# Optimization experiments

Hardware: AMD Instinct MI355X
Metric: run time of the kernel (lower is better)

Reference implementation:

```python
import jax, jax.numpy as jnp
import numpy as np

H, V, B, S = 2048, 32000, 16, 256

def setup_inputs() -> dict:
    key = jax.random.key(0)
    k1, k2, k3, k4 = jax.random.split(key, 4)
    # Parameters exactly as the torch __init__ builds them
    alpha_exp = jax.nn.softmax(jax.random.normal(k1, (H, H), dtype=jnp.float32), axis=1)   # transition probs [H,H]
    beta = jax.nn.log_softmax(jax.random.normal(k2, (H, V), dtype=jnp.float32), axis=1)    # emission log-probs [H,V]
    gamma = jax.nn.log_softmax(jax.random.normal(k3, (H,), dtype=jnp.float32), axis=0)     # initial-state logits [H]
    input_ids = jax.random.randint(k4, (B, S), 0, V)
    return {"input_ids": input_ids, "alpha_exp": alpha_exp, "beta": beta, "gamma": gamma}


def _hmm_forward(input_ids, alpha_exp, beta, gamma):
    # gamma stored as log-probs; forward re-softmaxes it (faithful to torch code)
    gamma_exp = jax.nn.softmax(gamma)                       # [H]
    ids = input_ids.T                                       # [S,B]
    mask = (ids != -1).astype(beta.dtype)                   # [S,B]; -1 = padding
    # input_probs[t,h,b] = beta[h, ids[t,b]] * mask
    ip = jnp.transpose(beta[:, ids], (1, 0, 2)) * mask[:, None, :]   # [S,H,B]
    ip_rev = ip[::-1]                                       # process t = S-1 .. 0

    def step(y, ipt):
        # log-domain backward recursion: y' = log(alpha_exp @ exp(y - ymax)) + ymax + emission
        ymax = jnp.max(y, axis=0, keepdims=True)            # [1,B]
        y = jnp.log(alpha_exp @ jnp.exp(y - ymax)) + ymax + ipt
        return y, y

    y0 = ip_rev[0]                                          # t = S-1: y starts at 0, += emission
    y_last, ys_rest = jax.lax.scan(step, y0, ip_rev[1:])
    ys = jnp.concatenate([y0[None], ys_rest], axis=0)       # [S,H,B], ys[i] is t = S-1-i

    ymax = jnp.max(y_last, axis=0)                          # [B]
    final = jnp.log(gamma_exp @ jnp.exp(y_last - ymax[None, :])) + ymax   # [B] per-seq loglik
    return ys, final


def reference(input_ids, alpha_exp, beta, gamma):
    return _hmm_forward(input_ids, alpha_exp, beta, gamma)
```

## Files before the change

### kernel.cpp

```cpp
#include <hip/hip_runtime.h>
#include <cstdint>
#include <cstddef>

#define Hh 2048
#define Vv 32000
#define Bb 16
#define Ss 256

typedef unsigned short ushort_t;
typedef unsigned int   uint_t;
typedef unsigned long long ull_t;

typedef __attribute__((ext_vector_type(8))) short short8;
typedef __attribute__((ext_vector_type(4))) float f32x4;

#define Z_OFF    0ull
#define Z_SLOT   ((size_t)Bb * Hh * 2)
#define Z_BYTES  ((size_t)3 * Z_SLOT)
#define Y_OFF    (Z_OFF + Z_BYTES)
#define Y_BYTES  ((size_t)Bb * Hh * 4)
#define WS_NEED  (Y_OFF + Y_BYTES)

#define LD_REL(p)     __hip_atomic_load((p), __ATOMIC_RELAXED, __HIP_MEMORY_SCOPE_AGENT)
#define ST_REL(p, v)  __hip_atomic_store((p), (v), __ATOMIC_RELAXED, __HIP_MEMORY_SCOPE_AGENT)

#define SGN64 0x8000800080008000ull
#define MAG64 0x7FFF7FFF7FFF7FFFull

__device__ __forceinline__ float b2f_u(uint_t u) {
  union { uint_t u; float f; } x; x.u = u; return x.f;
}
__device__ __forceinline__ ushort_t f2b(float f) {
  union { float f; uint_t u; } x; x.f = f;
  uint_t u = x.u;
  return (ushort_t)((u + 0x7FFFu + ((u >> 16) & 1u)) >> 16);
}
__device__ __forceinline__ uint_t umaxu(uint_t a, uint_t b) { return a > b ? a : b; }
__device__ __forceinline__ uint_t pkmax16(uint_t a, uint_t b) {
  uint_t lo = umaxu(a & 0xFFFFu, b & 0xFFFFu);
  uint_t hi = umaxu(a >> 16, b >> 16);
  return lo | (hi << 16);
}

__global__ __launch_bounds__(256, 1) void hmm_persist(
    const float* __restrict__ alpha,
    const float* __restrict__ beta,
    const int*  __restrict__ ids,
    ushort_t* __restrict__ Zbuf,
    float* __restrict__ Y255,
    float* __restrict__ out)
{
  const int w    = blockIdx.x;
  const int g    = w & 7;
  const int wl   = w >> 3;
  const int c0   = g * 2;
  const int tid  = threadIdx.x;
  const int wv   = tid >> 6;
  const int lane = tid & 63;
  const int lrow = lane & 15;
  const int quad = lane >> 4;
  const int r0   = wl * 64 + wv * 16;

  __shared__ __align__(16) ushort_t zTf[2 * 2080];
  __shared__ float ybuf[128];
  __shared__ float ipld[128];
  __shared__ uint_t redm[4];

  ull_t*  Zb64 = (ull_t*)Zbuf;
  uint_t* Zb32 = (uint_t*)Zbuf;

  short8 afr[64];
  {
    const float* arow = alpha + (size_t)(r0 + lrow) * Hh + quad * 8;
    #pragma unroll
    for (int kt = 0; kt < 64; ++kt) {
      float4 f0 = *(const float4*)(arow + kt * 32);
      float4 f1 = *(const float4*)(arow + kt * 32 + 4);
      short8 fr;
      fr[0] = (short)f2b(f0.x); fr[1] = (short)f2b(f0.y);
      fr[2] = (short)f2b(f0.z); fr[3] = (short)f2b(f0.w);
      fr[4] = (short)f2b(f1.x); fr[5] = (short)f2b(f1.y);
      fr[6] = (short)f2b(f1.z); fr[7] = (short)f2b(f1.w);
      afr[kt] = fr;
    }
  }

  const int myc = tid & 1;
  const int myr = wl * 64 + (tid >> 1);
  float ipreg = 0.f;

  {
    float yv = 0.f;
    if (tid < 128) {
      const int v = ids[(c0 + myc) * Ss + (Ss - 1)];
      yv = beta[(size_t)myr * Vv + v];
      ybuf[tid] = yv;
      out[(size_t)myr * Bb + (c0 + myc)] = yv;
    }
    __syncthreads();
    if (tid < 64) {
      const int c = tid >> 5, rr0 = (tid & 31) * 2;
      uint_t lo = f2b(__expf(ybuf[rr0 * 2 + c]));
      uint_t hi = f2b(__expf(ybuf[rr0 * 2 + 2 + c]));
      ST_REL(Zb32 + (size_t)(c0 + c) * 1024 + (wl * 32 + (tid & 31)),
             lo | (hi << 16));
    }
    if (tid < 128) {
      const int v1 = ids[(c0 + myc) * Ss + (Ss - 2)];
      ipreg = beta[(size_t)myr * Vv + v1];
    }
  }

  float mprev = 0.f;
  const ushort_t* zbase = zTf + (lrow & 1) * 2080 + quad * 8;

  for (int k = 1; k < Ss; ++k) {
    const int   physR = (3 - ((k - 1) % 3)) % 3;
    const ull_t expS  = ((k - 1) & 1) ? SGN64 : 0ull;

    ull_t zr[4];
    ull_t* zp[4];
    #pragma unroll
    for (int j = 0; j < 4; ++j) {
      const int idx = j * 256 + tid;
      const int c   = idx >> 9;
      const int h4  = idx & 511;
      zp[j] = Zb64 + (size_t)physR * (Bb * 512) + (size_t)(c0 + c) * 512 + h4;
      zr[j] = LD_REL(zp[j]);
    }
    while (true) {
      int bad = 0;
      #pragma unroll
      for (int j = 0; j < 4; ++j)
        if ((zr[j] & SGN64) != expS) bad |= (1 << j);
      if (!bad) break;
      #pragma unroll
      for (int j = 0; j < 4; ++j)
        if (bad & (1 << j)) zr[j] = LD_REL(zp[j]);
    }

    uint_t mloc[2] = {0u, 0u};
    #pragma unroll
    for (int j = 0; j < 4; ++j) {
      const ull_t v = zr[j] & MAG64;
      const int idx = j * 256 + tid;
      const int c   = idx >> 9;
      const int h   = (idx & 511) * 4;
      *(ull_t*)(zTf + c * 2080 + h) = v;
      uint_t a = (uint_t)v, b = (uint_t)(v >> 32);
      uint_t m2 = pkmax16(a, b);
      mloc[j >> 1] = umaxu(mloc[j >> 1], umaxu(m2 & 0xFFFFu, m2 >> 16));
    }
    if (tid < 128) ipld[tid] = ipreg;

    uint_t pk = mloc[0] | (mloc[1] << 16);
    #pragma unroll
    for (int d = 1; d < 64; d <<= 1)
      pk = pkmax16(pk, __shfl_xor(pk, d));
    if (lane == 0) redm[wv] = pk;
    __syncthreads();

    const uint_t rr  = pkmax16(pkmax16(redm[0], redm[1]),
                               pkmax16(redm[2], redm[3]));
    const uint_t mzb = (((lrow & 1) ? (rr >> 16) : (rr & 0xFFFFu)) << 16);
    const float  lmax = __logf(b2f_u(mzb));

    if (k < Ss - 1 && tid < 128) {
      const int v = ids[(c0 + myc) * Ss + (Ss - 2 - k)];
      ipreg = beta[(size_t)myr * Vv + v];
    }

    f32x4 acc[8];
    {
      f32x4 zv = {0.f, 0.f, 0.f, 0.f};
      #pragma unroll
      for (int j = 0; j < 8; ++j) acc[j] = zv;
    }
    #pragma unroll
    for (int kt = 0; kt < 64; ++kt) {
      short8 bfr = *(const short8*)(zbase + kt * 32);
      acc[kt & 7] = __builtin_amdgcn_mfma_f32_16x16x32_bf16(afr[kt], bfr, acc[kt & 7], 0, 0, 0);
    }
    f32x4 sf = ((acc[0] + acc[1]) + (acc[2] + acc[3])) +
               ((acc[4] + acc[5]) + (acc[6] + acc[7]));

    const int  c   = lrow;
    const int  rb  = r0 + quad * 4;
    const int  lrr = wv * 16 + quad * 4;
    const bool act = (lrow < 2);
    const int   physW = (3 - (k % 3)) % 3;
    const ull_t orS   = (k & 1) ? SGN64 : 0ull;
    const float mnew  = mprev + lmax;
    if (act) {
      float yv4[4];
      #pragma unroll
      for (int i = 0; i < 4; ++i)
        yv4[i] = __logf(sf[i]) + mprev + ipld[(lrr + i) * 2 + c];
      uint_t o0 = (uint_t)f2b(__expf(yv4[0] - mnew)) |
                  ((uint_t)f2b(__expf(yv4[1] - mnew)) << 16);
      uint_t o1 = (uint_t)f2b(__expf(yv4[2] - mnew)) |
                  ((uint_t)f2b(__expf(yv4[3] - mnew)) << 16);
      ST_REL(Zb64 + (size_t)physW * (Bb * 512) + (size_t)(c0 + c) * 512 + (rb >> 2),
             ((ull_t)o0 | ((ull_t)o1 << 32)) | orS);
      #pragma unroll
      for (int i = 0; i < 4; ++i)
        out[(size_t)k * (Hh * Bb) + (size_t)(rb + i) * Bb + (c0 + c)] = yv4[i];
      if (k == Ss - 1) {
        float4 yo; yo.x = yv4[0]; yo.y = yv4[1]; yo.z = yv4[2]; yo.w = yv4[3];
        *(float4*)(Y255 + (size_t)(c0 + c) * Hh + rb) = yo;
      }
    }
    mprev = mnew;
    __syncthreads();
  }
}

__global__ __launch_bounds__(256) void final_k(
    const float* __restrict__ gamma, const float* __restrict__ Y255,
    float* __restrict__ out)
{
  const int b = blockIdx.x;
  const int tid = threadIdx.x;
  __shared__ float sb[256];

  float ym = -3.0e38f;
  for (int h = tid; h < Hh; h += 256) ym = fmaxf(ym, Y255[(size_t)b * Hh + h]);
  sb[tid] = ym; __syncthreads();
  for (int off = 128; off; off >>= 1) {
    if (tid < off) sb[tid] = fmaxf(sb[tid], sb[tid + off]);
    __syncthreads();
  }
  ym = sb[0]; __syncthreads();

  float gm = -3.0e38f;
  for (int h = tid; h < Hh; h += 256) gm = fmaxf(gm, gamma[h]);
  sb[tid] = gm; __syncthreads();
  for (int off = 128; off; off >>= 1) {
    if (tid < off) sb[tid] = fmaxf(sb[tid], sb[tid + off]);
    __syncthreads();
  }
  gm = sb[0]; __syncthreads();

  float s1 = 0.f, s2 = 0.f;
  for (int h = tid; h < Hh; h += 256) {
    float gv = gamma[h] - gm;
    s1 += __expf(gv);
    s2 += __expf(gv + Y255[(size_t)b * Hh + h] - ym);
  }
  sb[tid] = s1; __syncthreads();
  for (int off = 128; off; off >>= 1) {
    if (tid < off) sb[tid] += sb[tid + off];
    __syncthreads();
  }
  s1 = sb[0]; __syncthreads();
  sb[tid] = s2; __syncthreads();
  for (int off = 128; off; off >>= 1) {
    if (tid < off) sb[tid] += sb[tid + off];
    __syncthreads();
  }
  s2 = sb[0];

  if (tid == 0)
    out[(size_t)Ss * Hh * Bb + b] = __logf(s2) - __logf(s1) + ym;
}

extern "C" void kernel_launch(void* const* d_in, const int* in_sizes, int n_in,
                              void* d_out, int out_size, void* d_ws, size_t ws_size,
                              hipStream_t stream) {
  (void)in_sizes; (void)n_in; (void)out_size;
  const int*   ids   = (const int*)d_in[0];
  const float* alpha = (const float*)d_in[1];
  const float* beta  = (const float*)d_in[2];
  const float* gamma = (const float*)d_in[3];
  float* out = (float*)d_out;
  char* ws = (char*)d_ws;

  if (ws_size < WS_NEED) return;

  ushort_t* Zbuf = (ushort_t*)(ws + Z_OFF);
  float*    Y255 = (float*)(ws + Y_OFF);

  hipMemsetAsync(ws + Z_OFF, 0x80, 2 * Z_SLOT, stream);
  hipMemsetAsync(ws + Z_OFF + 2 * Z_SLOT, 0x00, Z_SLOT, stream);

  {
    const float* a_alpha = alpha;
    const float* a_beta  = beta;
    const int*   a_ids   = ids;
    ushort_t* a_z = Zbuf;  float* a_y = Y255;  float* a_out = out;
    void* args[] = {(void*)&a_alpha, (void*)&a_beta, (void*)&a_ids,
                    (void*)&a_z, (void*)&a_y, (void*)&a_out};
    hipError_t e = hipLaunchCooperativeKernel((const void*)hmm_persist,
                                              dim3(256), dim3(256), args, 0, stream);
    if (e != hipSuccess) {
      hipLaunchKernelGGL(hmm_persist, dim3(256), dim3(256), 0, stream,
                         alpha, beta, ids, Zbuf, Y255, out);
    }
  }

  hipLaunchKernelGGL(final_k, dim3(Bb), dim3(256), 0, stream, gamma, Y255, out);
}
```

Measured before the change: 1.607 ms.

## Repartition persistent HMM kernel to 32 workgroups covering all batch columns with split-K

The persistent kernel drops from 256 workgroups (8 batch groups × 32 row blocks, 2 columns each) to 32 workgroups that each own 64 rows for all 16 batch columns. Each wave computes a K-slice of 512, and partial sums are reduced through shared memory. This lets the 16x16 MFMA tile use all 16 columns instead of wasting 14 of them, and cuts the number of workgroups polling the global flag buffer each step. In exchange it uses far fewer CUs, adds an extra shared-memory reduction barrier, and has each thread load 32 global words per step.

Measured after the change: 2.250 ms. +40.0%, slower.

```diff
diff --git a/kernel.cpp b/kernel.cpp
--- a/kernel.cpp
+++ b/kernel.cpp
@@ -6,6 +6,7 @@
 #define Vv 32000
 #define Bb 16
 #define Ss 256
+#define NWG 32
 
 typedef unsigned short ushort_t;
 typedef unsigned int   uint_t;
@@ -26,6 +27,8 @@
 
 #define SGN64 0x8000800080008000ull
 #define MAG64 0x7FFF7FFF7FFF7FFFull
+
+#define ZSTR 2056
 
 __device__ __forceinline__ float b2f_u(uint_t u) {
   union { uint_t u; float f; } x; x.u = u; return x.f;
@@ -50,168 +53,192 @@
     float* __restrict__ Y255,
     float* __restrict__ out)
 {
-  const int w    = blockIdx.x;
-  const int g    = w & 7;
-  const int wl   = w >> 3;
-  const int c0   = g * 2;
+  const int wl   = blockIdx.x;
   const int tid  = threadIdx.x;
   const int wv   = tid >> 6;
   const int lane = tid & 63;
   const int lrow = lane & 15;
   const int quad = lane >> 4;
-  const int r0   = wl * 64 + wv * 16;
-
-  __shared__ __align__(16) ushort_t zTf[2 * 2080];
-  __shared__ float ybuf[128];
-  __shared__ float ipld[128];
-  __shared__ uint_t redm[4];
-
-  ull_t*  Zb64 = (ull_t*)Zbuf;
-  uint_t* Zb32 = (uint_t*)Zbuf;
+
+  __shared__ __align__(16) ushort_t zTf[16 * ZSTR];
+  __shared__ float ipld[64 * 17];
+  __shared__ __align__(16) float red[4][4][256];
+  __shared__ uint_t mbuf[4][8];
+
+  ull_t* Zb64 = (ull_t*)Zbuf;
 
   short8 afr[64];
-  {
-    const float* arow = alpha + (size_t)(r0 + lrow) * Hh + quad * 8;
-    #pragma unroll
-    for (int kt = 0; kt < 64; ++kt) {
-      float4 f0 = *(const float4*)(arow + kt * 32);
-      float4 f1 = *(const float4*)(arow + kt * 32 + 4);
+  #pragma unroll
+  for (int t = 0; t < 4; ++t) {
+    #pragma unroll
+    for (int kt = 0; kt < 16; ++kt) {
+      const float* arow = alpha + (size_t)(wl * 64 + t * 16 + lrow) * Hh
+                          + wv * 512 + kt * 32 + quad * 8;
+      float4 f0 = *(const float4*)arow;
+      float4 f1 = *(const float4*)(arow + 4);
       short8 fr;
       fr[0] = (short)f2b(f0.x); fr[1] = (short)f2b(f0.y);
       fr[2] = (short)f2b(f0.z); fr[3] = (short)f2b(f0.w);
       fr[4] = (short)f2b(f1.x); fr[5] = (short)f2b(f1.y);
       fr[6] = (short)f2b(f1.z); fr[7] = (short)f2b(f1.w);
-      afr[kt] = fr;
-    }
-  }
-
-  const int myc = tid & 1;
-  const int myr = wl * 64 + (tid >> 1);
-  float ipreg = 0.f;
+      afr[t * 16 + kt] = fr;
+    }
+  }
+
+  const int cg = tid & 15;
+  const int r4 = tid >> 4;
+  float ipreg[4];
 
   {
-    float yv = 0.f;
-    if (tid < 128) {
-      const int v = ids[(c0 + myc) * Ss + (Ss - 1)];
-      yv = beta[(size_t)myr * Vv + v];
-      ybuf[tid] = yv;
-      out[(size_t)myr * Bb + (c0 + myc)] = yv;
-    }
-    __syncthreads();
-    if (tid < 64) {
-      const int c = tid >> 5, rr0 = (tid & 31) * 2;
-      uint_t lo = f2b(__expf(ybuf[rr0 * 2 + c]));
-      uint_t hi = f2b(__expf(ybuf[rr0 * 2 + 2 + c]));
-      ST_REL(Zb32 + (size_t)(c0 + c) * 1024 + (wl * 32 + (tid & 31)),
-             lo | (hi << 16));
-    }
-    if (tid < 128) {
-      const int v1 = ids[(c0 + myc) * Ss + (Ss - 2)];
-      ipreg = beta[(size_t)myr * Vv + v1];
-    }
+    const int ci = tid >> 4, gi = tid & 15;
+    const int h0 = (wl * 16 + gi) * 4;
+    const int v  = ids[ci * Ss + (Ss - 1)];
+    float y0 = beta[(size_t)(h0 + 0) * Vv + v];
+    float y1 = beta[(size_t)(h0 + 1) * Vv + v];
+    float y2 = beta[(size_t)(h0 + 2) * Vv + v];
+    float y3 = beta[(size_t)(h0 + 3) * Vv + v];
+    out[(size_t)(h0 + 0) * Bb + ci] = y0;
+    out[(size_t)(h0 + 1) * Bb + ci] = y1;
+    out[(size_t)(h0 + 2) * Bb + ci] = y2;
+    out[(size_t)(h0 + 3) * Bb + ci] = y3;
+    uint_t o0 = (uint_t)f2b(__expf(y0)) | ((uint_t)f2b(__expf(y1)) << 16);
+    uint_t o1 = (uint_t)f2b(__expf(y2)) | ((uint_t)f2b(__expf(y3)) << 16);
+    ST_REL(Zb64 + (size_t)ci * 512 + (wl * 16 + gi),
+           (ull_t)o0 | ((ull_t)o1 << 32));
+    const int v1 = ids[cg * Ss + (Ss - 2)];
+    #pragma unroll
+    for (int i = 0; i < 4; ++i)
+      ipreg[i] = beta[(size_t)(wl * 64 + r4 * 4 + i) * Vv + v1];
   }
 
   float mprev = 0.f;
-  const ushort_t* zbase = zTf + (lrow & 1) * 2080 + quad * 8;
 
   for (int k = 1; k < Ss; ++k) {
     const int   physR = (3 - ((k - 1) % 3)) % 3;
     const ull_t expS  = ((k - 1) & 1) ? SGN64 : 0ull;
 
-    ull_t zr[4];
-    ull_t* zp[4];
-    #pragma unroll
-    for (int j = 0; j < 4; ++j) {
-      const int idx = j * 256 + tid;
-      const int c   = idx >> 9;
-      const int h4  = idx & 511;
-      zp[j] = Zb64 + (size_t)physR * (Bb * 512) + (size_t)(c0 + c) * 512 + h4;
-      zr[j] = LD_REL(zp[j]);
-    }
-    while (true) {
-      int bad = 0;
-      #pragma unroll
-      for (int j = 0; j < 4; ++j)
-        if ((zr[j] & SGN64) != expS) bad |= (1 << j);
-      if (!bad) break;
-      #pragma unroll
-      for (int j = 0; j < 4; ++j)
-        if (bad & (1 << j)) zr[j] = LD_REL(zp[j]);
-    }
-
-    uint_t mloc[2] = {0u, 0u};
-    #pragma unroll
-    for (int j = 0; j < 4; ++j) {
-      const ull_t v = zr[j] & MAG64;
-      const int idx = j * 256 + tid;
-      const int c   = idx >> 9;
-      const int h   = (idx & 511) * 4;
-      *(ull_t*)(zTf + c * 2080 + h) = v;
-      uint_t a = (uint_t)v, b = (uint_t)(v >> 32);
-      uint_t m2 = pkmax16(a, b);
-      mloc[j >> 1] = umaxu(mloc[j >> 1], umaxu(m2 & 0xFFFFu, m2 >> 16));
-    }
-    if (tid < 128) ipld[tid] = ipreg;
-
-    uint_t pk = mloc[0] | (mloc[1] << 16);
-    #pragma unroll
-    for (int d = 1; d < 64; d <<= 1)
-      pk = pkmax16(pk, __shfl_xor(pk, d));
-    if (lane == 0) redm[wv] = pk;
-    __syncthreads();
-
-    const uint_t rr  = pkmax16(pkmax16(redm[0], redm[1]),
-                               pkmax16(redm[2], redm[3]));
-    const uint_t mzb = (((lrow & 1) ? (rr >> 16) : (rr & 0xFFFFu)) << 16);
-    const float  lmax = __logf(b2f_u(mzb));
-
-    if (k < Ss - 1 && tid < 128) {
-      const int v = ids[(c0 + myc) * Ss + (Ss - 2 - k)];
-      ipreg = beta[(size_t)myr * Vv + v];
-    }
-
-    f32x4 acc[8];
+    ull_t za[16], zb[16];
     {
-      f32x4 zv = {0.f, 0.f, 0.f, 0.f};
-      #pragma unroll
-      for (int j = 0; j < 8; ++j) acc[j] = zv;
-    }
-    #pragma unroll
-    for (int kt = 0; kt < 64; ++kt) {
-      short8 bfr = *(const short8*)(zbase + kt * 32);
-      acc[kt & 7] = __builtin_amdgcn_mfma_f32_16x16x32_bf16(afr[kt], bfr, acc[kt & 7], 0, 0, 0);
-    }
-    f32x4 sf = ((acc[0] + acc[1]) + (acc[2] + acc[3])) +
-               ((acc[4] + acc[5]) + (acc[6] + acc[7]));
-
-    const int  c   = lrow;
-    const int  rb  = r0 + quad * 4;
-    const int  lrr = wv * 16 + quad * 4;
-    const bool act = (lrow < 2);
+      ull_t* base = Zb64 + (size_t)physR * 8192 + 2 * (size_t)tid;
+      #pragma unroll
+      for (int j = 0; j < 16; ++j) {
+        za[j] = LD_REL(base + j * 512);
+        zb[j] = LD_REL(base + j * 512 + 1);
+      }
+      while (true) {
+        bool ok = true;
+        #pragma unroll
+        for (int j = 0; j < 16; ++j) {
+          if ((za[j] & SGN64) != expS) ok = false;
+          if ((zb[j] & SGN64) != expS) ok = false;
+        }
+        if (ok) break;
+        #pragma unroll
+        for (int j = 0; j < 16; ++j) {
+          if ((za[j] & SGN64) != expS) za[j] = LD_REL(base + j * 512);
+          if ((zb[j] & SGN64) != expS) zb[j] = LD_REL(base + j * 512 + 1);
+        }
+      }
+    }
+
+    uint_t pk[8];
+    {
+      uint_t cm[16];
+      #pragma unroll
+      for (int j = 0; j < 16; ++j) {
+        const ull_t a = za[j] & MAG64, b = zb[j] & MAG64;
+        uint4 w4;
+        w4.x = (uint_t)a; w4.y = (uint_t)(a >> 32);
+        w4.z = (uint_t)b; w4.w = (uint_t)(b >> 32);
+        *(uint4*)(zTf + j * ZSTR + tid * 8) = w4;
+        uint_t m = pkmax16(pkmax16(w4.x, w4.y), pkmax16(w4.z, w4.w));
+        cm[j] = umaxu(m & 0xFFFFu, m >> 16);
+      }
+      #pragma unroll
+      for (int i = 0; i < 8; ++i) pk[i] = cm[2 * i] | (cm[2 * i + 1] << 16);
+      #pragma unroll
+      for (int d = 1; d < 64; d <<= 1) {
+        #pragma unroll
+        for (int i = 0; i < 8; ++i)
+          pk[i] = pkmax16(pk[i], (uint_t)__shfl_xor((int)pk[i], d));
+      }
+      if (lane == 0) {
+        #pragma unroll
+        for (int i = 0; i < 8; ++i) mbuf[wv][i] = pk[i];
+      }
+      #pragma unroll
+      for (int i = 0; i < 4; ++i)
+        ipld[(r4 * 4 + i) * 17 + cg] = ipreg[i];
+    }
+    __syncthreads();
+
+    float ipv[4];
+    #pragma unroll
+    for (int i = 0; i < 4; ++i)
+      ipv[i] = ipld[(wv * 16 + quad * 4 + i) * 17 + lrow];
+    uint_t mm;
+    {
+      uint_t v0 = mbuf[0][lrow >> 1], v1 = mbuf[1][lrow >> 1];
+      uint_t v2 = mbuf[2][lrow >> 1], v3 = mbuf[3][lrow >> 1];
+      uint_t mpk = pkmax16(pkmax16(v0, v1), pkmax16(v2, v3));
+      mm = (lrow & 1) ? (mpk >> 16) : (mpk & 0xFFFFu);
+    }
+    const float lmax = __logf(b2f_u(mm << 16));
+
+    if (k < Ss - 1) {
+      const int v = ids[cg * Ss + (Ss - 2 - k)];
+      #pragma unroll
+      for (int i = 0; i < 4; ++i)
+        ipreg[i] = beta[(size_t)(wl * 64 + r4 * 4 + i) * Vv + v];
+    }
+
+    f32x4 acc[4];
+    {
+      f32x4 z4 = {0.f, 0.f, 0.f, 0.f};
+      acc[0] = z4; acc[1] = z4; acc[2] = z4; acc[3] = z4;
+    }
+    const ushort_t* zb_l = zTf + lrow * ZSTR + wv * 512 + quad * 8;
+    #pragma unroll
+    for (int kt = 0; kt < 16; ++kt) {
+      short8 bfr = *(const short8*)(zb_l + kt * 32);
+      #pragma unroll
+      for (int t = 0; t < 4; ++t)
+        acc[t] = __builtin_amdgcn_mfma_f32_16x16x32_bf16(afr[t * 16 + kt], bfr, acc[t], 0, 0, 0);
+    }
+
+    #pragma unroll
+    for (int t = 0; t < 4; ++t)
+      if (t != wv) *(f32x4*)&red[t][wv][lane * 4] = acc[t];
+    __syncthreads();
+    f32x4 sf = acc[0];
+    if (wv == 1) sf = acc[1];
+    else if (wv == 2) sf = acc[2];
+    else if (wv == 3) sf = acc[3];
+    #pragma unroll
+    for (int v = 0; v < 4; ++v)
+      if (v != wv) sf += *(const f32x4*)&red[wv][v][lane * 4];
+
+    const float mnew = mprev + lmax;
+    float yv[4];
+    #pragma unroll
+    for (int i = 0; i < 4; ++i)
+      yv[i] = __logf(sf[i]) + mprev + ipv[i];
+    uint_t o0 = (uint_t)f2b(__expf(yv[0] - mnew)) |
+                ((uint_t)f2b(__expf(yv[1] - mnew)) << 16);
+    uint_t o1 = (uint_t)f2b(__expf(yv[2] - mnew)) |
+                ((uint_t)f2b(__expf(yv[3] - mnew)) << 16);
     const int   physW = (3 - (k % 3)) % 3;
     const ull_t orS   = (k & 1) ? SGN64 : 0ull;
-    const float mnew  = mprev + lmax;
-    if (act) {
-      float yv4[4];
-      #pragma unroll
-      for (int i = 0; i < 4; ++i)
-        yv4[i] = __logf(sf[i]) + mprev + ipld[(lrr + i) * 2 + c];
-      uint_t o0 = (uint_t)f2b(__expf(yv4[0] - mnew)) |
-                  ((uint_t)f2b(__expf(yv4[1] - mnew)) << 16);
-      uint_t o1 = (uint_t)f2b(__expf(yv4[2] - mnew)) |
-                  ((uint_t)f2b(__expf(yv4[3] - mnew)) << 16);
-      ST_REL(Zb64 + (size_t)physW * (Bb * 512) + (size_t)(c0 + c) * 512 + (rb >> 2),
-             ((ull_t)o0 | ((ull_t)o1 << 32)) | orS);
-      #pragma unroll
-      for (int i = 0; i < 4; ++i)
-        out[(size_t)k * (Hh * Bb) + (size_t)(rb + i) * Bb + (c0 + c)] = yv4[i];
-      if (k == Ss - 1) {
-        float4 yo; yo.x = yv4[0]; yo.y = yv4[1]; yo.z = yv4[2]; yo.w = yv4[3];
-        *(float4*)(Y255 + (size_t)(c0 + c) * Hh + rb) = yo;
-      }
+    ST_REL(Zb64 + (size_t)physW * 8192 + (size_t)lrow * 512 + (wl * 16 + wv * 4 + quad),
+           ((ull_t)o0 | ((ull_t)o1 << 32)) | orS);
+    #pragma unroll
+    for (int i = 0; i < 4; ++i)
+      out[(size_t)k * (Hh * Bb) + (size_t)(wl * 64 + wv * 16 + quad * 4 + i) * Bb + lrow] = yv[i];
+    if (k == Ss - 1) {
+      float4 yo; yo.x = yv[0]; yo.y = yv[1]; yo.z = yv[2]; yo.w = yv[3];
+      *(float4*)(Y255 + (size_t)lrow * Hh + (wl * 64 + wv * 16 + quad * 4)) = yo;
     }
     mprev = mnew;
-    __syncthreads();
   }
 }
 
@@ -291,9 +318,9 @@
     void* args[] = {(void*)&a_alpha, (void*)&a_beta, (void*)&a_ids,
                     (void*)&a_z, (void*)&a_y, (void*)&a_out};
     hipError_t e = hipLaunchCooperativeKernel((const void*)hmm_persist,
-                                              dim3(256), dim3(256), args, 0, stream);
+                                              dim3(NWG), dim3(256), args, 0, stream);
     if (e != hipSuccess) {
-      hipLaunchKernelGGL(hmm_persist, dim3(256), dim3(256), 0, stream,
+      hipLaunchKernelGGL(hmm_persist, dim3(NWG), dim3(256), 0, stream,
                          alpha, beta, ids, Zbuf, Y255, out);
     }
   }
```
